# Kernel optimization log

Hardware: AMD Instinct MI355X
Metric: run time of the kernel (lower is better)

Reference implementation:

```python
import jax, jax.numpy as jnp
import numpy as np

B, L, D, H, OUT = 4, 2048, 1024, 8, 256
DH = D // H
EPS = 1e-12


def setup_inputs() -> dict:
    key = jax.random.key(0)
    ks = jax.random.split(key, 20)
    s = lambda fan_in: 1.0 / np.sqrt(fan_in)
    def lin(k, fin, fout):
        k1, k2 = jax.random.split(k)
        w = jax.random.uniform(k1, (fin, fout), jnp.float32, -s(fin), s(fin))
        b = jax.random.uniform(k2, (fout,), jnp.float32, -s(fin), s(fin))
        return w, b
    x = jax.random.normal(ks[0], (B, L, D), jnp.float32)
    wq, bq = lin(ks[1], D, D)
    wk, bk = lin(ks[2], D, D)
    wv, bv = lin(ks[3], D, D)
    gamma = jnp.ones((D,), jnp.float32)
    beta = jnp.zeros((D,), jnp.float32)
    wff, bff = lin(ks[4], D, D)
    wc1, bc1 = lin(ks[5], D, D)
    wc2, bc2 = lin(ks[6], D, 1)
    wl1, bl1 = lin(ks[7], L, L)
    wl2, bl2 = lin(ks[8], L, OUT)
    return dict(x=x, wq=wq, bq=bq, wk=wk, bk=bk, wv=wv, bv=bv,
                gamma=gamma, beta=beta, wff=wff, bff=bff,
                wc1=wc1, bc1=bc1, wc2=wc2, bc2=bc2,
                wl1=wl1, bl1=bl1, wl2=wl2, bl2=bl2)


def layernorm(x, gamma, beta):
    mean = x.mean(-1, keepdims=True)
    var = ((x - mean) ** 2).mean(-1, keepdims=True)  # biased variance
    return gamma * (x - mean) / jnp.sqrt(var + EPS) + beta


def reference(x, wq, bq, wk, bk, wv, bv, gamma, beta, wff, bff,
              wc1, bc1, wc2, bc2, wl1, bl1, wl2, bl2):
    # multi-head self-attention (dropout = identity at inference)
    q = (x @ wq + bq).reshape(B, L, H, DH)
    k = (x @ wk + bk).reshape(B, L, H, DH)
    v = (x @ wv + bv).reshape(B, L, H, DH)
    scores = jnp.einsum('bqhd,bkhd->bhqk', q, k) / np.sqrt(DH)
    attn = jax.nn.softmax(scores, axis=-1)                  # [B,H,L,L]
    ctx = jnp.einsum('bhqk,bkhd->bqhd', attn, v).reshape(B, L, D)
    h = layernorm(x + ctx, gamma, beta)
    # feedforward: Linear + ReLU (hidden = d_model), residual + same layernorm params
    ff = jax.nn.relu(h @ wff + bff)
    h = layernorm(h + ff, gamma, beta)
    # collapse d_model -> 1
    c = jax.nn.relu(h @ wc1 + bc1)
    c = jax.nn.relu(c @ wc2 + bc2)                          # [B,L,1]
    c = jnp.squeeze(c, axis=-1)                             # [B,L]
    # collapse length -> out_featuresize
    c = jax.nn.relu(c @ wl1 + bl1)
    out = c @ wl2 + bl2                                     # [B,OUT]
    return out
```

## Files before the change

### kernel.cpp

```cpp
#include <hip/hip_runtime.h>

typedef unsigned short u16;
typedef unsigned int u32;
typedef __attribute__((ext_vector_type(4))) float f32x4;
typedef __attribute__((ext_vector_type(8))) short short8;
typedef __attribute__((ext_vector_type(4))) u32 u32x4;
typedef __attribute__((ext_vector_type(4))) u16 u16x4;

#define BB 4
#define LL 2048
#define DD 1024
#define HH 8
#define DHH 128

__device__ __forceinline__ u16 f2b(float f) {
  u32 u = __builtin_bit_cast(u32, f);
  u += 0x7fffu + ((u >> 16) & 1u);
  return (u16)(u >> 16);
}
__device__ __forceinline__ float b2f(u16 h) {
  u32 u = ((u32)h) << 16;
  return __builtin_bit_cast(float, u);
}
__device__ __forceinline__ float exp2_fast(float x) {
  float r;
  asm("v_exp_f32 %0, %1" : "=v"(r) : "v"(x));
  return r;
}

#define GLDS16(g, l)                                                          \
  __builtin_amdgcn_global_load_lds(                                           \
      (const __attribute__((address_space(1))) void*)(g),                     \
      (__attribute__((address_space(3))) void*)(l), 16, 0, 0)

__global__ __launch_bounds__(256) void cvt_k(const float* __restrict__ X,
                                             u16* __restrict__ Xb, long n) {
  long i = ((long)blockIdx.x * 256 + threadIdx.x) * 4;
  if (i >= n) return;
  f32x4 v = *(const f32x4*)(X + i);
  u16x4 o;
#pragma unroll
  for (int k = 0; k < 4; k++) o[k] = f2b(v[k]);
  *(u16x4*)(Xb + i) = o;
}

__global__ __launch_bounds__(256) void tr_k(const float* __restrict__ W,
                                            u16* __restrict__ WT) {
  __shared__ float tile[32][33];
  const int bx = blockIdx.x, by = blockIdx.y;
  const int tx = threadIdx.x & 31, ty = threadIdx.x >> 5;
#pragma unroll
  for (int i = 0; i < 4; i++)
    tile[ty + i * 8][tx] =
        W[(long)(by * 32 + ty + i * 8) * 1024 + bx * 32 + tx];
  __syncthreads();
#pragma unroll
  for (int i = 0; i < 4; i++)
    WT[(long)(bx * 32 + ty + i * 8) * 1024 + by * 32 + tx] =
        f2b(tile[tx][ty + i * 8]);
}

template <bool RELU, int OMODE>
__global__ __launch_bounds__(256, 2) void gemm_k(
    const u16* __restrict__ A, const u16* __restrict__ BT,
    const float* __restrict__ bias, float scale, float* __restrict__ Cf,
    u16* __restrict__ Cb, int M, int N, int K) {
  __shared__ u16 As[128 * 32];
  __shared__ u16 Bs[128 * 32];
  const int nwg = gridDim.x * gridDim.y;
  const int bid = blockIdx.x + blockIdx.y * gridDim.x;
  const int swz = (bid & 7) * (nwg >> 3) + (bid >> 3);
  const int bxi = swz % gridDim.x, byi = swz / gridDim.x;
  const int t = threadIdx.x;
  const int l = t & 63, w = t >> 6;
  const int lr = l & 15, lg = l >> 4;
  const int wr = (w >> 1) * 64, wc = (w & 1) * 64;
  const long bm = (long)byi * 128, bn = (long)bxi * 128;
  const int srow = l >> 2;
  const int scol = (l & 3) * 8;
  const u16* Ag0 = A + (bm + w * 32 + srow) * (long)K + scol;
  const u16* Ag1 = A + (bm + w * 32 + 16 + srow) * (long)K + scol;
  const u16* Bg0 = BT + (bn + w * 32 + srow) * (long)K + scol;
  const u16* Bg1 = BT + (bn + w * 32 + 16 + srow) * (long)K + scol;
  u16* Al0 = As + w * 1024;
  u16* Al1 = As + w * 1024 + 512;
  u16* Bl0 = Bs + w * 1024;
  u16* Bl1 = Bs + w * 1024 + 512;
  f32x4 acc[4][4] = {};
  for (int k0 = 0; k0 < K; k0 += 32) {
    GLDS16(Ag0 + k0, Al0);
    GLDS16(Ag1 + k0, Al1);
    GLDS16(Bg0 + k0, Bl0);
    GLDS16(Bg1 + k0, Bl1);
    __syncthreads();
    short8 af[4], bf[4];
#pragma unroll
    for (int i = 0; i < 4; i++)
      af[i] = *(const short8*)&As[(wr + i * 16 + lr) * 32 + lg * 8];
#pragma unroll
    for (int i = 0; i < 4; i++)
      bf[i] = *(const short8*)&Bs[(wc + i * 16 + lr) * 32 + lg * 8];
#pragma unroll
    for (int i = 0; i < 4; i++)
#pragma unroll
      for (int j = 0; j < 4; j++)
        acc[i][j] = __builtin_amdgcn_mfma_f32_16x16x32_bf16(af[i], bf[j],
                                                            acc[i][j], 0, 0, 0);
    __syncthreads();
  }
#pragma unroll
  for (int i = 0; i < 4; i++)
#pragma unroll
    for (int j = 0; j < 4; j++) {
      long col = bn + wc + j * 16 + lr;
      float bv = bias[col];
      if (OMODE == 2) {
        long row0 = bm + wr + i * 16 + lg * 4;
        long b = row0 >> 11, l0 = row0 & 2047;
        u16x4 ov;
#pragma unroll
        for (int r = 0; r < 4; r++) {
          float v2 = (acc[i][j][r] + bv) * scale;
          if (RELU) v2 = fmaxf(v2, 0.f);
          ov[r] = f2b(v2);
        }
        *(u16x4*)(Cb + (b * 1024 + col) * 2048 + l0) = ov;
      } else {
#pragma unroll
        for (int r = 0; r < 4; r++) {
          long row = bm + wr + i * 16 + lg * 4 + r;
          float v2 = (acc[i][j][r] + bv) * scale;
          if (RELU) v2 = fmaxf(v2, 0.f);
          if (OMODE == 1)
            Cb[row * N + col] = f2b(v2);
          else
            Cf[row * N + col] = v2;
        }
      }
    }
}

__global__ __launch_bounds__(512, 4) void flash_k(const u16* __restrict__ Q,
                                                  const u16* __restrict__ Kb,
                                                  const u16* __restrict__ VT,
                                                  float* __restrict__ ctx) {
  __shared__ u16 Ks[64][136];
  __shared__ u16 VTs[128][72];
  __shared__ u16 Pw[8][16][76];
  const int nwg = gridDim.x * gridDim.y;
  const int bid = blockIdx.x + blockIdx.y * gridDim.x;
  const int swz = (bid & 7) * (nwg >> 3) + (bid >> 3);
  const int bxi = swz % gridDim.x, byi = swz / gridDim.x;
  const int t = threadIdx.x;
  const int l = t & 63, w = t >> 6;
  const int lr = l & 15, lg = l >> 4;
  const int b = byi >> 3, h = byi & 7;
  const long kbase = ((long)b * LL) * DD + h * DHH;
  const long vtbase = ((long)(b * 8 + h) * DHH) * LL;
  const int q0 = bxi * 128;

  short8 qf[4];
  {
    const u16* qp = Q + kbase + (long)(q0 + w * 16 + lr) * DD + lg * 8;
#pragma unroll
    for (int c = 0; c < 4; c++) qf[c] = *(const short8*)(qp + c * 32);
  }
  f32x4 oacc[8] = {};
  float mprev[4] = {-1e30f, -1e30f, -1e30f, -1e30f};
  float lsum[4] = {0.f, 0.f, 0.f, 0.f};

  const int krow = t >> 3, kcol = (t & 7) * 16;
  const int vrow = t >> 2, vcol = (t & 3) * 16;
  u32x4 kr0, kr1, vr0, vr1;
  {
    const u16* kp = Kb + kbase + (long)krow * DD + kcol;
    kr0 = *(const u32x4*)(kp);
    kr1 = *(const u32x4*)(kp + 8);
    const u16* vp = VT + vtbase + (long)vrow * LL + vcol;
    vr0 = *(const u32x4*)(vp);
    vr1 = *(const u32x4*)(vp + 8);
  }
  for (int kb = 0; kb < LL; kb += 64) {
    *(u32x4*)&Ks[krow][kcol] = kr0;
    *(u32x4*)&Ks[krow][kcol + 8] = kr1;
    *(u32x4*)&VTs[vrow][vcol] = vr0;
    *(u32x4*)&VTs[vrow][vcol + 8] = vr1;
    __syncthreads();
    if (kb + 64 < LL) {
      const u16* kp = Kb + kbase + (long)(kb + 64 + krow) * DD + kcol;
      kr0 = *(const u32x4*)(kp);
      kr1 = *(const u32x4*)(kp + 8);
      const u16* vp = VT + vtbase + (long)vrow * LL + kb + 64 + vcol;
      vr0 = *(const u32x4*)(vp);
      vr1 = *(const u32x4*)(vp + 8);
    }

    f32x4 s[4] = {};
#pragma unroll
    for (int jc = 0; jc < 4; jc++)
#pragma unroll
      for (int c = 0; c < 4; c++) {
        short8 kf = *(const short8*)&Ks[jc * 16 + lr][c * 32 + lg * 8];
        s[jc] =
            __builtin_amdgcn_mfma_f32_16x16x32_bf16(qf[c], kf, s[jc], 0, 0, 0);
      }

    float mnew[4];
    bool need = false;
#pragma unroll
    for (int r = 0; r < 4; r++) {
      float mx = fmaxf(fmaxf(s[0][r], s[1][r]), fmaxf(s[2][r], s[3][r]));
      mx = fmaxf(mx, __shfl_xor(mx, 1, 64));
      mx = fmaxf(mx, __shfl_xor(mx, 2, 64));
      mx = fmaxf(mx, __shfl_xor(mx, 4, 64));
      mx = fmaxf(mx, __shfl_xor(mx, 8, 64));
      mnew[r] = mx;
      need = need || (mx > mprev[r] + 8.f);
    }
    if (__any((int)need)) {
#pragma unroll
      for (int r = 0; r < 4; r++) {
        float mn = fmaxf(mprev[r], mnew[r]);
        float alpha = exp2_fast(mprev[r] - mn);
        mprev[r] = mn;
        lsum[r] *= alpha;
#pragma unroll
        for (int d8 = 0; d8 < 8; d8++) oacc[d8][r] *= alpha;
      }
    }
    float rs[4] = {0.f, 0.f, 0.f, 0.f};
#pragma unroll
    for (int jc = 0; jc < 4; jc++)
#pragma unroll
      for (int r = 0; r < 4; r++) {
        float p = exp2_fast(s[jc][r] - mprev[r]);
        rs[r] += p;
        Pw[w][lg * 4 + r][jc * 16 + lr] = f2b(p);
      }
#pragma unroll
    for (int r = 0; r < 4; r++) {
      rs[r] += __shfl_xor(rs[r], 1, 64);
      rs[r] += __shfl_xor(rs[r], 2, 64);
      rs[r] += __shfl_xor(rs[r], 4, 64);
      rs[r] += __shfl_xor(rs[r], 8, 64);
      lsum[r] += rs[r];
    }

#pragma unroll
    for (int kk = 0; kk < 2; kk++) {
      short8 pf = *(const short8*)&Pw[w][lr][kk * 32 + lg * 8];
#pragma unroll
      for (int d8 = 0; d8 < 8; d8++) {
        short8 vf = *(const short8*)&VTs[d8 * 16 + lr][kk * 32 + lg * 8];
        oacc[d8] =
            __builtin_amdgcn_mfma_f32_16x16x32_bf16(pf, vf, oacc[d8], 0, 0, 0);
      }
    }
    __syncthreads();
  }
#pragma unroll
  for (int r = 0; r < 4; r++) {
    float inv = 1.f / lsum[r];
    float* cp = ctx + kbase + (long)(q0 + w * 16 + lg * 4 + r) * DD;
#pragma unroll
    for (int d8 = 0; d8 < 8; d8++) cp[d8 * 16 + lr] = oacc[d8][r] * inv;
  }
}

__global__ __launch_bounds__(256) void ln_k(const float* __restrict__ X,
                                            const float* __restrict__ R,
                                            const float* __restrict__ gamma,
                                            const float* __restrict__ beta,
                                            float* __restrict__ Hf,
                                            u16* __restrict__ Hb) {
  const int row = blockIdx.x, t = threadIdx.x;
  const long off = (long)row * DD + t * 4;
  f32x4 v = *(const f32x4*)(X + off);
  f32x4 rv = *(const f32x4*)(R + off);
#pragma unroll
  for (int i = 0; i < 4; i++) v[i] += rv[i];
  float s = v[0] + v[1] + v[2] + v[3];
  float q = v[0] * v[0] + v[1] * v[1] + v[2] * v[2] + v[3] * v[3];
#pragma unroll
  for (int m = 32; m >= 1; m >>= 1) {
    s += __shfl_xor(s, m, 64);
    q += __shfl_xor(q, m, 64);
  }
  __shared__ float red[8];
  if ((t & 63) == 0) {
    red[t >> 6] = s;
    red[4 + (t >> 6)] = q;
  }
  __syncthreads();
  s = red[0] + red[1] + red[2] + red[3];
  q = red[4] + red[5] + red[6] + red[7];
  const float mean = s * (1.f / 1024.f);
  const float var = q * (1.f / 1024.f) - mean * mean;
  const float rstd = rsqrtf(var + 1e-12f);
  f32x4 g = *(const f32x4*)(gamma + t * 4);
  f32x4 be = *(const f32x4*)(beta + t * 4);
  f32x4 o;
#pragma unroll
  for (int i = 0; i < 4; i++) o[i] = g[i] * (v[i] - mean) * rstd + be[i];
  if (Hf) *(f32x4*)(Hf + off) = o;
  if (Hb) {
    u16x4 ob;
#pragma unroll
    for (int i = 0; i < 4; i++) ob[i] = f2b(o[i]);
    *(u16x4*)(Hb + off) = ob;
  }
}

__global__ __launch_bounds__(256) void c2_k(const u16* __restrict__ C,
                                            const float* __restrict__ wc2,
                                            const float* __restrict__ bc2,
                                            float* __restrict__ cvec) {
  const int row = blockIdx.x, t = threadIdx.x;
  u16x4 cv = *(const u16x4*)(C + (long)row * DD + t * 4);
  f32x4 wv = *(const f32x4*)(wc2 + t * 4);
  float s = b2f(cv[0]) * wv[0] + b2f(cv[1]) * wv[1] + b2f(cv[2]) * wv[2] +
            b2f(cv[3]) * wv[3];
#pragma unroll
  for (int m = 32; m >= 1; m >>= 1) s += __shfl_xor(s, m, 64);
  __shared__ float red[4];
  if ((t & 63) == 0) red[t >> 6] = s;
  __syncthreads();
  if (t == 0)
    cvec[row] = fmaxf(red[0] + red[1] + red[2] + red[3] + bc2[0], 0.f);
}

__global__ __launch_bounds__(256) void smm_part(const float* __restrict__ Cin,
                                                const float* __restrict__ W,
                                                float* __restrict__ P, int Lr,
                                                int N, int SL) {
  const int j = blockIdx.x * 256 + threadIdx.x;
  const int l0 = blockIdx.y * SL;
  float a0 = 0, a1 = 0, a2 = 0, a3 = 0;
  for (int ll = l0; ll < l0 + SL; ll++) {
    float wv = W[(long)ll * N + j];
    a0 += Cin[ll] * wv;
    a1 += Cin[Lr + ll] * wv;
    a2 += Cin[2 * Lr + ll] * wv;
    a3 += Cin[3 * Lr + ll] * wv;
  }
  float* Pp = P + ((long)blockIdx.y * 4) * N + j;
  Pp[0] = a0;
  Pp[N] = a1;
  Pp[2 * N] = a2;
  Pp[3 * N] = a3;
}

template <bool RELU>
__global__ __launch_bounds__(256) void smm_red(const float* __restrict__ P,
                                               const float* __restrict__ bias,
                                               float* __restrict__ Out, int N,
                                               int S) {
  const int j = blockIdx.x * 256 + threadIdx.x;
#pragma unroll
  for (int b = 0; b < 4; b++) {
    float a = 0;
    for (int s = 0; s < S; s++) a += P[((long)s * 4 + b) * N + j];
    a += bias[j];
    if (RELU) a = fmaxf(a, 0.f);
    Out[(long)b * N + j] = a;
  }
}

extern "C" void kernel_launch(void* const* d_in, const int* in_sizes, int n_in,
                              void* d_out, int out_size, void* d_ws,
                              size_t ws_size, hipStream_t stream) {
  (void)in_sizes; (void)n_in; (void)out_size; (void)ws_size;
  const float* x = (const float*)d_in[0];
  const float* wq = (const float*)d_in[1];
  const float* bq = (const float*)d_in[2];
  const float* wk = (const float*)d_in[3];
  const float* bk = (const float*)d_in[4];
  const float* wv = (const float*)d_in[5];
  const float* bv = (const float*)d_in[6];
  const float* gamma = (const float*)d_in[7];
  const float* beta = (const float*)d_in[8];
  const float* wff = (const float*)d_in[9];
  const float* bff = (const float*)d_in[10];
  const float* wc1 = (const float*)d_in[11];
  const float* bc1 = (const float*)d_in[12];
  const float* wc2 = (const float*)d_in[13];
  const float* bc2 = (const float*)d_in[14];
  const float* wl1 = (const float*)d_in[15];
  const float* bl1 = (const float*)d_in[16];
  const float* wl2 = (const float*)d_in[17];
  const float* bl2 = (const float*)d_in[18];

  char* wsp = (char*)d_ws;
  size_t off = 0;
  auto take = [&](size_t bytes) -> char* {
    char* p = wsp + off;
    off += (bytes + 255) & ~(size_t)255;
    return p;
  };
  u16* xb = (u16*)take((size_t)8192 * 1024 * 2);
  u16* wqT = (u16*)take((size_t)1024 * 1024 * 2);
  u16* wkT = (u16*)take((size_t)1024 * 1024 * 2);
  u16* wvT = (u16*)take((size_t)1024 * 1024 * 2);
  u16* wffT = (u16*)take((size_t)1024 * 1024 * 2);
  u16* wc1T = (u16*)take((size_t)1024 * 1024 * 2);
  u16* qb = (u16*)take((size_t)8192 * 1024 * 2);
  u16* kbuf = (u16*)take((size_t)8192 * 1024 * 2);
  u16* vT = (u16*)take((size_t)8192 * 1024 * 2);
  float* ctxb = (float*)take((size_t)8192 * 1024 * 4);
  float* h1f = (float*)take((size_t)8192 * 1024 * 4);
  float* cvec = (float*)take(8192 * 4);
  float* c3 = (float*)take(8192 * 4);
  float* P1 = (float*)take((size_t)16 * 4 * 2048 * 4);
  float* P2 = (float*)take((size_t)16 * 4 * 256 * 4);
  u16* h1b = qb;
  u16* h2b = kbuf;
  u16* cb = vT;
  float* ff = ctxb;

  cvt_k<<<8192, 256, 0, stream>>>(x, xb, (long)8192 * 1024);
  dim3 trg(32, 32);
  tr_k<<<trg, 256, 0, stream>>>(wq, wqT);
  tr_k<<<trg, 256, 0, stream>>>(wk, wkT);
  tr_k<<<trg, 256, 0, stream>>>(wv, wvT);
  tr_k<<<trg, 256, 0, stream>>>(wff, wffT);
  tr_k<<<trg, 256, 0, stream>>>(wc1, wc1T);

  dim3 gg(8, 64);
  gemm_k<false, 1><<<gg, 256, 0, stream>>>(
      xb, wqT, bq, 0.12751743f, nullptr, qb, 8192, 1024, 1024);
  gemm_k<false, 1><<<gg, 256, 0, stream>>>(xb, wkT, bk, 1.f, nullptr, kbuf,
                                           8192, 1024, 1024);
  gemm_k<false, 2><<<gg, 256, 0, stream>>>(xb, wvT, bv, 1.f, nullptr, vT,
                                           8192, 1024, 1024);
  flash_k<<<dim3(16, 32), 512, 0, stream>>>(qb, kbuf, vT, ctxb);
  ln_k<<<8192, 256, 0, stream>>>(x, ctxb, gamma, beta, h1f, h1b);
  gemm_k<true, 0><<<gg, 256, 0, stream>>>(h1b, wffT, bff, 1.f, ff, nullptr,
                                          8192, 1024, 1024);
  ln_k<<<8192, 256, 0, stream>>>(h1f, ff, gamma, beta, nullptr, h2b);
  gemm_k<true, 1><<<gg, 256, 0, stream>>>(h2b, wc1T, bc1, 1.f, nullptr, cb,
                                          8192, 1024, 1024);
  c2_k<<<8192, 256, 0, stream>>>(cb, wc2, bc2, cvec);
  smm_part<<<dim3(8, 16), 256, 0, stream>>>(cvec, wl1, P1, 2048, 2048, 128);
  smm_red<true><<<8, 256, 0, stream>>>(P1, bl1, c3, 2048, 16);
  smm_part<<<dim3(1, 16), 256, 0, stream>>>(c3, wl2, P2, 2048, 256, 128);
  smm_red<false><<<1, 256, 0, stream>>>(P2, bl2, (float*)d_out, 256, 16);
}
```

Baseline: 429.7 us.

## Double-buffer K/V tiles and keep P in registers via transposed QK MFMA

The flash attention kernel now double-buffers the K and V^T shared-memory tiles, leaving one barrier per iteration where there were two. It also swaps the MFMA operand order so each lane holds the scores for a single query row. That turns the row max and sum reductions into two cross-lane shuffles and keeps one running max and sum per lane instead of four. The P tile is repacked into A-operand layout with ds_bpermute, removing the LDS round trip for P. In exchange it uses more shared memory per block, which may lower occupancy, and it adds bpermute and shuffle traffic for the alpha and lsum redistribution.

New measurement: 399.6 us. 7.0% less time.

```diff
diff --git a/kernel.cpp b/kernel.cpp
--- a/kernel.cpp
+++ b/kernel.cpp
@@ -26,6 +26,12 @@
   float r;
   asm("v_exp_f32 %0, %1" : "=v"(r) : "v"(x));
   return r;
+}
+__device__ __forceinline__ u32 packbf(float a, float b) {
+  return (u32)f2b(a) | ((u32)f2b(b) << 16);
+}
+__device__ __forceinline__ u32 bperm(int srcLane, u32 v) {
+  return (u32)__builtin_amdgcn_ds_bpermute(srcLane << 2, (int)v);
 }
 
 #define GLDS16(g, l)                                                          \
@@ -144,9 +150,8 @@
                                                   const u16* __restrict__ Kb,
                                                   const u16* __restrict__ VT,
                                                   float* __restrict__ ctx) {
-  __shared__ u16 Ks[64][136];
-  __shared__ u16 VTs[128][72];
-  __shared__ u16 Pw[8][16][76];
+  __shared__ u16 Ks[2][64][136];
+  __shared__ u16 VTs[2][128][72];
   const int nwg = gridDim.x * gridDim.y;
   const int bid = blockIdx.x + blockIdx.y * gridDim.x;
   const int swz = (bid & 7) * (nwg >> 3) + (bid >> 3);
@@ -166,8 +171,8 @@
     for (int c = 0; c < 4; c++) qf[c] = *(const short8*)(qp + c * 32);
   }
   f32x4 oacc[8] = {};
-  float mprev[4] = {-1e30f, -1e30f, -1e30f, -1e30f};
-  float lsum[4] = {0.f, 0.f, 0.f, 0.f};
+  float mprev = -1e30f;
+  float lsum = 0.f;
 
   const int krow = t >> 3, kcol = (t & 7) * 16;
   const int vrow = t >> 2, vcol = (t & 3) * 16;
@@ -179,88 +184,107 @@
     const u16* vp = VT + vtbase + (long)vrow * LL + vcol;
     vr0 = *(const u32x4*)(vp);
     vr1 = *(const u32x4*)(vp + 8);
-  }
-  for (int kb = 0; kb < LL; kb += 64) {
-    *(u32x4*)&Ks[krow][kcol] = kr0;
-    *(u32x4*)&Ks[krow][kcol + 8] = kr1;
-    *(u32x4*)&VTs[vrow][vcol] = vr0;
-    *(u32x4*)&VTs[vrow][vcol + 8] = vr1;
-    __syncthreads();
-    if (kb + 64 < LL) {
-      const u16* kp = Kb + kbase + (long)(kb + 64 + krow) * DD + kcol;
+    *(u32x4*)&Ks[0][krow][kcol] = kr0;
+    *(u32x4*)&Ks[0][krow][kcol + 8] = kr1;
+    *(u32x4*)&VTs[0][vrow][vcol] = vr0;
+    *(u32x4*)&VTs[0][vrow][vcol + 8] = vr1;
+  }
+  const int NT = LL / 64;
+  for (int it = 0; it < NT; ++it) {
+    const int cur = it & 1;
+    if (it + 1 < NT) {
+      const u16* kp = Kb + kbase + (long)((it + 1) * 64 + krow) * DD + kcol;
       kr0 = *(const u32x4*)(kp);
       kr1 = *(const u32x4*)(kp + 8);
-      const u16* vp = VT + vtbase + (long)vrow * LL + kb + 64 + vcol;
+      const u16* vp = VT + vtbase + (long)vrow * LL + (it + 1) * 64 + vcol;
       vr0 = *(const u32x4*)(vp);
       vr1 = *(const u32x4*)(vp + 8);
     }
+    __syncthreads();
 
     f32x4 s[4] = {};
 #pragma unroll
     for (int jc = 0; jc < 4; jc++)
 #pragma unroll
       for (int c = 0; c < 4; c++) {
-        short8 kf = *(const short8*)&Ks[jc * 16 + lr][c * 32 + lg * 8];
+        short8 kf = *(const short8*)&Ks[cur][jc * 16 + lr][c * 32 + lg * 8];
         s[jc] =
-            __builtin_amdgcn_mfma_f32_16x16x32_bf16(qf[c], kf, s[jc], 0, 0, 0);
+            __builtin_amdgcn_mfma_f32_16x16x32_bf16(kf, qf[c], s[jc], 0, 0, 0);
       }
 
-    float mnew[4];
-    bool need = false;
-#pragma unroll
-    for (int r = 0; r < 4; r++) {
-      float mx = fmaxf(fmaxf(s[0][r], s[1][r]), fmaxf(s[2][r], s[3][r]));
-      mx = fmaxf(mx, __shfl_xor(mx, 1, 64));
-      mx = fmaxf(mx, __shfl_xor(mx, 2, 64));
-      mx = fmaxf(mx, __shfl_xor(mx, 4, 64));
-      mx = fmaxf(mx, __shfl_xor(mx, 8, 64));
-      mnew[r] = mx;
-      need = need || (mx > mprev[r] + 8.f);
-    }
-    if (__any((int)need)) {
-#pragma unroll
-      for (int r = 0; r < 4; r++) {
-        float mn = fmaxf(mprev[r], mnew[r]);
-        float alpha = exp2_fast(mprev[r] - mn);
-        mprev[r] = mn;
-        lsum[r] *= alpha;
-#pragma unroll
-        for (int d8 = 0; d8 < 8; d8++) oacc[d8][r] *= alpha;
+    float mx = fmaxf(fmaxf(s[0][0], s[0][1]), fmaxf(s[0][2], s[0][3]));
+#pragma unroll
+    for (int jc = 1; jc < 4; jc++)
+      mx = fmaxf(mx, fmaxf(fmaxf(s[jc][0], s[jc][1]),
+                           fmaxf(s[jc][2], s[jc][3])));
+    mx = fmaxf(mx, __shfl_xor(mx, 16, 64));
+    mx = fmaxf(mx, __shfl_xor(mx, 32, 64));
+
+    if (__any((int)(mx > mprev + 8.f))) {
+      float mn = fmaxf(mprev, mx);
+      float alpha = exp2_fast(mprev - mn);
+      mprev = mn;
+      lsum *= alpha;
+      float ar[4];
+#pragma unroll
+      for (int r = 0; r < 4; r++) ar[r] = __shfl(alpha, lg * 4 + r, 64);
+#pragma unroll
+      for (int d8 = 0; d8 < 8; d8++)
+#pragma unroll
+        for (int r = 0; r < 4; r++) oacc[d8][r] *= ar[r];
+    }
+
+    u32 pk2[4][2];
+    float ladd = 0.f;
+#pragma unroll
+    for (int jc = 0; jc < 4; jc++) {
+      float p0 = exp2_fast(s[jc][0] - mprev);
+      float p1 = exp2_fast(s[jc][1] - mprev);
+      float p2 = exp2_fast(s[jc][2] - mprev);
+      float p3 = exp2_fast(s[jc][3] - mprev);
+      ladd += (p0 + p1) + (p2 + p3);
+      pk2[jc][0] = packbf(p0, p1);
+      pk2[jc][1] = packbf(p2, p3);
+    }
+    lsum += ladd;
+
+    short8 pf[2];
+#pragma unroll
+    for (int kk = 0; kk < 2; kk++) {
+      u32x4 afv;
+#pragma unroll
+      for (int m = 0; m < 4; m++) {
+        int srcl = lr + ((((lg & 1) << 1) + (m >> 1)) << 4);
+        u32 a0 = bperm(srcl, pk2[2 * kk][m & 1]);
+        u32 a1 = bperm(srcl, pk2[2 * kk + 1][m & 1]);
+        afv[m] = (lg >> 1) ? a1 : a0;
       }
-    }
-    float rs[4] = {0.f, 0.f, 0.f, 0.f};
-#pragma unroll
-    for (int jc = 0; jc < 4; jc++)
-#pragma unroll
-      for (int r = 0; r < 4; r++) {
-        float p = exp2_fast(s[jc][r] - mprev[r]);
-        rs[r] += p;
-        Pw[w][lg * 4 + r][jc * 16 + lr] = f2b(p);
+      pf[kk] = __builtin_bit_cast(short8, afv);
+    }
+
+#pragma unroll
+    for (int kk = 0; kk < 2; kk++)
+#pragma unroll
+      for (int d8 = 0; d8 < 8; d8++) {
+        short8 vf = *(const short8*)&VTs[cur][d8 * 16 + lr][kk * 32 + lg * 8];
+        oacc[d8] =
+            __builtin_amdgcn_mfma_f32_16x16x32_bf16(pf[kk], vf, oacc[d8], 0,
+                                                    0, 0);
       }
-#pragma unroll
-    for (int r = 0; r < 4; r++) {
-      rs[r] += __shfl_xor(rs[r], 1, 64);
-      rs[r] += __shfl_xor(rs[r], 2, 64);
-      rs[r] += __shfl_xor(rs[r], 4, 64);
-      rs[r] += __shfl_xor(rs[r], 8, 64);
-      lsum[r] += rs[r];
-    }
-
-#pragma unroll
-    for (int kk = 0; kk < 2; kk++) {
-      short8 pf = *(const short8*)&Pw[w][lr][kk * 32 + lg * 8];
-#pragma unroll
-      for (int d8 = 0; d8 < 8; d8++) {
-        short8 vf = *(const short8*)&VTs[d8 * 16 + lr][kk * 32 + lg * 8];
-        oacc[d8] =
-            __builtin_amdgcn_mfma_f32_16x16x32_bf16(pf, vf, oacc[d8], 0, 0, 0);
-      }
-    }
-    __syncthreads();
-  }
+
+    if (it + 1 < NT) {
+      *(u32x4*)&Ks[cur ^ 1][krow][kcol] = kr0;
+      *(u32x4*)&Ks[cur ^ 1][krow][kcol + 8] = kr1;
+      *(u32x4*)&VTs[cur ^ 1][vrow][vcol] = vr0;
+      *(u32x4*)&VTs[cur ^ 1][vrow][vcol + 8] = vr1;
+    }
+  }
+
+  lsum += __shfl_xor(lsum, 16, 64);
+  lsum += __shfl_xor(lsum, 32, 64);
 #pragma unroll
   for (int r = 0; r < 4; r++) {
-    float inv = 1.f / lsum[r];
+    float inv = 1.f / __shfl(lsum, lg * 4 + r, 64);
     float* cp = ctx + kbase + (long)(q0 + w * 16 + lg * 4 + r) * DD;
 #pragma unroll
     for (int d8 = 0; d8 < 8; d8++) cp[d8 * 16 + lr] = oacc[d8][r] * inv;
```
